# Performance work log

Measured on AMD Instinct MI355X. Metric: run time of the kernel, lower is better.

Reference implementation:

```python
import jax, jax.numpy as jnp
import numpy as np

N_NODES = 50000
N_EDGES = 800000


def setup_inputs() -> dict:
    key = jax.random.key(0)
    ks = jax.random.split(key, 8)
    feats = jax.random.normal(ks[0], (N_NODES, 256), dtype=jnp.float32)
    src = jax.random.randint(ks[1], (N_EDGES,), 0, N_NODES, dtype=jnp.int32)
    dst = jax.random.randint(ks[2], (N_EDGES,), 0, N_NODES, dtype=jnp.int32)
    # Glorot-ish init for GraphConv weights
    W0 = jax.random.normal(ks[3], (256, 256), dtype=jnp.float32) * (1.0 / 16.0)
    W1 = jax.random.normal(ks[4], (256, 256), dtype=jnp.float32) * (1.0 / 16.0)
    W2 = jax.random.normal(ks[5], (256, 128), dtype=jnp.float32) * (1.0 / 16.0)
    b0 = jnp.zeros((256,), dtype=jnp.float32)
    b1 = jnp.zeros((256,), dtype=jnp.float32)
    b2 = jnp.zeros((128,), dtype=jnp.float32)
    return {"feats": feats, "src": src, "dst": dst,
            "W0": W0, "b0": b0, "W1": W1, "b1": b1, "W2": W2, "b2": b2}


def _graph_conv(x, src, dst, W, b, activate):
    """DGL GraphConv with norm='both': h = D_in^{-1/2} A D_out^{-1/2} x W + b."""
    n = x.shape[0]
    e_ones = jnp.ones(src.shape[0], dtype=x.dtype)
    deg_out = jax.ops.segment_sum(e_ones, src, num_segments=n)  # out-degree (src norm)
    deg_in = jax.ops.segment_sum(e_ones, dst, num_segments=n)   # in-degree (dst norm)
    norm_src = jnp.where(deg_out > 0, deg_out, 1.0) ** -0.5
    norm_dst = jnp.where(deg_in > 0, deg_in, 1.0) ** -0.5
    h = x * norm_src[:, None]
    # transform first (in_feats >= out_feats path in DGL) then aggregate
    h = h @ W
    m = jax.ops.segment_sum(h[src], dst, num_segments=n)  # [N, out] neighbor sum
    h = m * norm_dst[:, None] + b
    if activate:
        h = jax.nn.relu(h)
    return h


def reference(feats, src, dst, W0, b0, W1, b1, W2, b2):
    # dropout is identity in eval mode
    h0 = _graph_conv(feats, src, dst, W0, b0, True)
    h1 = _graph_conv(h0, src, dst, W1, b1, True)
    h2 = _graph_conv(h1, src, dst, W2, b2, False)  # last layer: no activation
    return (h0, h1, h2, h2)  # (h_list..., h)
```

## Files before the change

### kernel.cpp

```cpp
#include <hip/hip_runtime.h>
#include <hip/hip_bf16.h>

#define NN 50000
#define NE 800000
#define MPAD 50048
#define BSTR 64

typedef __attribute__((ext_vector_type(8))) short short8;
typedef __attribute__((ext_vector_type(4))) float f32x4;
typedef __attribute__((ext_vector_type(4))) unsigned short us4;
typedef __attribute__((ext_vector_type(8))) unsigned short us8;

static __device__ __forceinline__ unsigned short f2bf(float f) {
    union { float f; unsigned int u; } v; v.f = f;
    unsigned int u = v.u;
    return (unsigned short)((u + 0x7FFFu + ((u >> 16) & 1u)) >> 16);
}
static __device__ __forceinline__ float bf2f(unsigned short h) {
    union { unsigned int u; float f; } v; v.u = ((unsigned int)h) << 16;
    return v.f;
}

__global__ void k_degsortW(const int* __restrict__ src, const int* __restrict__ dst,
                           int* __restrict__ degO, int* __restrict__ degI,
                           unsigned short* __restrict__ bucket,
                           const float* __restrict__ W0, const float* __restrict__ W1,
                           const float* __restrict__ W2,
                           unsigned short* __restrict__ W0T, unsigned short* __restrict__ W1T,
                           unsigned short* __restrict__ W2T) {
    int bid = blockIdx.x;
    int t = threadIdx.x;
    if (bid < NE / 256) {
        int e = bid * 256 + t;
        int s = src[e], d = dst[e];
        atomicAdd(&degO[s], 1);
        int p = atomicAdd(&degI[d], 1);
        bucket[d * BSTR + p] = (unsigned short)s;
    } else {
        int i = (bid - NE / 256) * 256 + t;
        if (i < 65536) {
            int k = i >> 8, c = i & 255;
            W0T[c * 256 + k] = f2bf(W0[i]);
        } else if (i < 131072) {
            int j = i - 65536;
            int k = j >> 8, c = j & 255;
            W1T[c * 256 + k] = f2bf(W1[j]);
        } else {
            int j = i - 131072;
            int k = j >> 7, c = j & 127;
            W2T[c * 256 + k] = f2bf(W2[j]);
        }
    }
}

__global__ __launch_bounds__(256) void k_prep(const float* __restrict__ x,
                                              const int* __restrict__ degO,
                                              const int* __restrict__ degI,
                                              float* __restrict__ nS, float* __restrict__ nD,
                                              unsigned short* __restrict__ xb) {
    const int row = blockIdx.x * 4 + (threadIdx.x >> 6);
    const int l = threadIdx.x & 63;
    int o = degO[row];
    float ns = 1.0f / sqrtf((float)(o > 0 ? o : 1));
    if (l == 0) {
        int d = degI[row];
        nS[row] = ns;
        nD[row] = 1.0f / sqrtf((float)(d > 0 ? d : 1));
    }
    f32x4 v = *(const f32x4*)&x[(long)row * 256 + l * 4];
    us4 ob;
#pragma unroll
    for (int k = 0; k < 4; k++) ob[k] = f2bf(v[k] * ns);
    *(us4*)&xb[(long)row * 256 + l * 4] = ob;
}

__global__ __launch_bounds__(256) void k_aggb(const int* __restrict__ degI,
                                              const unsigned short* __restrict__ bucket,
                                              const unsigned short* __restrict__ xb,
                                              const float* __restrict__ nD,
                                              unsigned short* __restrict__ aggb) {
    const int node = blockIdx.x * 4 + (threadIdx.x >> 6);
    const int lane = threadIdx.x & 63;
    const int q = lane >> 4;
    const int cl = (lane & 15) * 16;
    if (node >= NN) {
        if (node < MPAD && q == 0) {
            us8 z = {0,0,0,0,0,0,0,0};
            *(us8*)&aggb[(long)node * 256 + cl] = z;
            *(us8*)&aggb[(long)node * 256 + cl + 8] = z;
        }
        return;
    }
    const int deg = degI[node];
    const int bidx = (int)bucket[node * BSTR + lane];
    float acc[16];
#pragma unroll
    for (int k = 0; k < 16; k++) acc[k] = 0.f;
    int j = 0;
    for (; j + 8 <= deg; j += 8) {
        int s0 = __shfl(bidx, j + q, 64);
        int s1 = __shfl(bidx, j + 4 + q, 64);
        const unsigned short* g0 = &xb[(long)s0 * 256 + cl];
        const unsigned short* g1 = &xb[(long)s1 * 256 + cl];
        us8 a0 = *(const us8*)g0;
        us8 a1 = *(const us8*)(g0 + 8);
        us8 b0 = *(const us8*)g1;
        us8 b1 = *(const us8*)(g1 + 8);
#pragma unroll
        for (int k = 0; k < 8; k++) {
            acc[k]     += bf2f(a0[k]) + bf2f(b0[k]);
            acc[8 + k] += bf2f(a1[k]) + bf2f(b1[k]);
        }
    }
    if (j + 4 <= deg) {
        int s0 = __shfl(bidx, j + q, 64);
        const unsigned short* g0 = &xb[(long)s0 * 256 + cl];
        us8 a0 = *(const us8*)g0;
        us8 a1 = *(const us8*)(g0 + 8);
#pragma unroll
        for (int k = 0; k < 8; k++) { acc[k] += bf2f(a0[k]); acc[8 + k] += bf2f(a1[k]); }
        j += 4;
    }
    if (j < deg) {
        int s0 = __shfl(bidx, j + q, 64);
        if (q < deg - j) {
            const unsigned short* g0 = &xb[(long)s0 * 256 + cl];
            us8 a0 = *(const us8*)g0;
            us8 a1 = *(const us8*)(g0 + 8);
#pragma unroll
            for (int k = 0; k < 8; k++) { acc[k] += bf2f(a0[k]); acc[8 + k] += bf2f(a1[k]); }
        }
    }
#pragma unroll
    for (int k = 0; k < 16; k++) acc[k] += __shfl_xor(acc[k], 16, 64);
#pragma unroll
    for (int k = 0; k < 16; k++) acc[k] += __shfl_xor(acc[k], 32, 64);
    if (q == 0) {
        float nd = nD[node];
        us8 o0, o1;
#pragma unroll
        for (int k = 0; k < 8; k++) {
            o0[k] = f2bf(acc[k] * nd);
            o1[k] = f2bf(acc[8 + k] * nd);
        }
        *(us8*)&aggb[(long)node * 256 + cl] = o0;
        *(us8*)&aggb[(long)node * 256 + cl + 8] = o1;
    }
}

template<int NOUT, int MODE>
__global__ __launch_bounds__(256) void k_gemm(const unsigned short* __restrict__ A,
                                              const unsigned short* __restrict__ BT,
                                              const float* __restrict__ bias,
                                              const float* __restrict__ nS,
                                              float* __restrict__ outF,
                                              unsigned short* __restrict__ xbn,
                                              unsigned short* __restrict__ outB) {
    __shared__ unsigned short As[128][40];
    __shared__ unsigned short Bs[128][36];
    const int bm = blockIdx.x * 128;
    const int bn = blockIdx.y * 128;
    const int tid = threadIdx.x;
    const int lane = tid & 63;
    const int w = tid >> 6;
    const int wr = w >> 1, wc = w & 1;

    f32x4 acc[4][4];
#pragma unroll
    for (int m = 0; m < 4; m++)
#pragma unroll
        for (int n = 0; n < 4; n++) acc[m][n] = (f32x4){0.f, 0.f, 0.f, 0.f};

    for (int kt = 0; kt < 256; kt += 32) {
        {
            int r = tid >> 1, c = (tid & 1) * 16;
            const unsigned short* g = &A[(long)(bm + r) * 256 + kt + c];
            *(us8*)&As[r][c]     = *(const us8*)(g);
            *(us8*)&As[r][c + 8] = *(const us8*)(g + 8);
        }
        {
            int col = tid >> 1, kh = (tid & 1) * 16;
            const unsigned short* g = &BT[(long)(bn + col) * 256 + kt + kh];
            *(us8*)&Bs[col][kh]     = *(const us8*)(g);
            *(us8*)&Bs[col][kh + 8] = *(const us8*)(g + 8);
        }
        __syncthreads();

        union U { us4 h[2]; short8 s; };
        const int kb = (lane >> 4) * 4;
        short8 af[4], bf[4];
#pragma unroll
        for (int m = 0; m < 4; m++) {
            int r = wr * 64 + m * 16 + (lane & 15);
            U u; u.h[0] = *(const us4*)&As[r][kb]; u.h[1] = *(const us4*)&As[r][kb + 16];
            af[m] = u.s;
        }
#pragma unroll
        for (int n = 0; n < 4; n++) {
            int cl = wc * 64 + n * 16 + (lane & 15);
            U u; u.h[0] = *(const us4*)&Bs[cl][kb]; u.h[1] = *(const us4*)&Bs[cl][kb + 16];
            bf[n] = u.s;
        }
#pragma unroll
        for (int m = 0; m < 4; m++)
#pragma unroll
            for (int n = 0; n < 4; n++)
                acc[m][n] = __builtin_amdgcn_mfma_f32_16x16x32_bf16(af[m], bf[n], acc[m][n], 0, 0, 0);
        __syncthreads();
    }

#pragma unroll
    for (int m = 0; m < 4; m++) {
        int rbase = bm + wr * 64 + m * 16 + (lane >> 4) * 4;
        float ns[4];
        bool in[4];
        if (MODE == 0) {
#pragma unroll
            for (int j = 0; j < 4; j++) {
                int row = rbase + j;
                in[j] = row < NN;
                ns[j] = in[j] ? nS[row] : 0.f;
            }
        }
#pragma unroll
        for (int n = 0; n < 4; n++) {
            int gc = bn + wc * 64 + n * 16 + (lane & 15);
            float bb = (MODE == 0) ? bias[gc] : 0.f;
#pragma unroll
            for (int j = 0; j < 4; j++) {
                int row = rbase + j;
                if (MODE == 0) {
                    if (in[j]) {
                        float v = fmaxf(acc[m][n][j] + bb, 0.f);
                        __builtin_nontemporal_store(v, &outF[(long)row * 256 + gc]);
                        xbn[(long)row * 256 + gc] = f2bf(v * ns[j]);
                    } else {
                        xbn[(long)row * 256 + gc] = 0;
                    }
                } else {
                    outB[(long)row * NOUT + gc] = f2bf(acc[m][n][j]);
                }
            }
        }
    }
}

__global__ __launch_bounds__(256) void k_agg2(const int* __restrict__ degI,
                                              const unsigned short* __restrict__ bucket,
                                              const unsigned short* __restrict__ hgb,
                                              const float* __restrict__ nD,
                                              const float* __restrict__ b,
                                              float* __restrict__ h2,
                                              float* __restrict__ h2b) {
    const int node = blockIdx.x * 4 + (threadIdx.x >> 6);
    const int lane = threadIdx.x & 63;
    if (node >= NN) return;
    const int q = lane >> 4;
    const int cl = (lane & 15) * 8;
    const int deg = degI[node];
    const int bidx = (int)bucket[node * BSTR + lane];
    float acc[8];
#pragma unroll
    for (int k = 0; k < 8; k++) acc[k] = 0.f;
    int j = 0;
    for (; j + 8 <= deg; j += 8) {
        int s0 = __shfl(bidx, j + q, 64);
        int s1 = __shfl(bidx, j + 4 + q, 64);
        us8 vA = *(const us8*)&hgb[(long)s0 * 128 + cl];
        us8 vB = *(const us8*)&hgb[(long)s1 * 128 + cl];
#pragma unroll
        for (int k = 0; k < 8; k++) acc[k] += bf2f(vA[k]) + bf2f(vB[k]);
    }
    if (j + 4 <= deg) {
        int s0 = __shfl(bidx, j + q, 64);
        us8 vA = *(const us8*)&hgb[(long)s0 * 128 + cl];
#pragma unroll
        for (int k = 0; k < 8; k++) acc[k] += bf2f(vA[k]);
        j += 4;
    }
    if (j < deg) {
        int s0 = __shfl(bidx, j + q, 64);
        if (q < deg - j) {
            us8 vA = *(const us8*)&hgb[(long)s0 * 128 + cl];
#pragma unroll
            for (int k = 0; k < 8; k++) acc[k] += bf2f(vA[k]);
        }
    }
#pragma unroll
    for (int k = 0; k < 8; k++) acc[k] += __shfl_xor(acc[k], 16, 64);
#pragma unroll
    for (int k = 0; k < 8; k++) acc[k] += __shfl_xor(acc[k], 32, 64);
    if (q == 0) {
        float nd = nD[node];
        f32x4 v0, v1;
#pragma unroll
        for (int k = 0; k < 4; k++) v0[k] = acc[k] * nd + b[cl + k];
#pragma unroll
        for (int k = 0; k < 4; k++) v1[k] = acc[4 + k] * nd + b[cl + 4 + k];
        __builtin_nontemporal_store(v0, (f32x4*)&h2[(long)node * 128 + cl]);
        __builtin_nontemporal_store(v1, (f32x4*)&h2[(long)node * 128 + cl + 4]);
        __builtin_nontemporal_store(v0, (f32x4*)&h2b[(long)node * 128 + cl]);
        __builtin_nontemporal_store(v1, (f32x4*)&h2b[(long)node * 128 + cl + 4]);
    }
}

extern "C" void kernel_launch(void* const* d_in, const int* in_sizes, int n_in,
                              void* d_out, int out_size, void* d_ws, size_t ws_size,
                              hipStream_t stream) {
    const float* feats = (const float*)d_in[0];
    const int*   src   = (const int*)d_in[1];
    const int*   dst   = (const int*)d_in[2];
    const float* W0 = (const float*)d_in[3];
    const float* b0 = (const float*)d_in[4];
    const float* W1 = (const float*)d_in[5];
    const float* b1 = (const float*)d_in[6];
    const float* W2 = (const float*)d_in[7];
    const float* b2 = (const float*)d_in[8];

    float* out = (float*)d_out;
    float* h0  = out;
    float* h1  = out + (long)NN * 256;
    float* h2  = out + 2L * NN * 256;
    float* h2b = out + 2L * NN * 256 + (long)NN * 128;

    char* ws = (char*)d_ws;
    size_t off = 0;
    auto alloc = [&](size_t bytes) { void* p = ws + off; off += (bytes + 255) & ~255UL; return p; };
    unsigned short* xb   = (unsigned short*)alloc((size_t)MPAD * 256 * 2);
    unsigned short* xb2  = (unsigned short*)alloc((size_t)MPAD * 256 * 2);
    unsigned short* aggb = (unsigned short*)alloc((size_t)MPAD * 256 * 2);
    unsigned short* hgb  = (unsigned short*)alloc((size_t)MPAD * 128 * 2);
    unsigned short* W0T = (unsigned short*)alloc(256 * 256 * 2);
    unsigned short* W1T = (unsigned short*)alloc(256 * 256 * 2);
    unsigned short* W2T = (unsigned short*)alloc(128 * 256 * 2);
    int*   zint   = (int*)alloc((size_t)2 * NN * 4);
    int*   degO   = zint;
    int*   degI   = zint + NN;
    float* nS     = (float*)alloc(NN * 4);
    float* nD     = (float*)alloc(NN * 4);
    unsigned short* bucket = (unsigned short*)alloc((size_t)NN * BSTR * 2);

    hipMemsetAsync(zint, 0, (size_t)2 * NN * 4, stream);
    k_degsortW<<<NE / 256 + 640, 256, 0, stream>>>(src, dst, degO, degI, bucket,
                                                   W0, W1, W2, W0T, W1T, W2T);

    k_prep<<<NN / 4, 256, 0, stream>>>(feats, degO, degI, nS, nD, xb);

    k_aggb<<<MPAD / 4, 256, 0, stream>>>(degI, bucket, xb, nD, aggb);
    k_gemm<256, 0><<<dim3(MPAD / 128, 2), 256, 0, stream>>>(aggb, W0T, b0, nS, h0, xb2, nullptr);

    k_aggb<<<MPAD / 4, 256, 0, stream>>>(degI, bucket, xb2, nD, aggb);
    k_gemm<256, 0><<<dim3(MPAD / 128, 2), 256, 0, stream>>>(aggb, W1T, b1, nS, h1, xb, nullptr);

    k_gemm<128, 1><<<dim3(MPAD / 128, 1), 256, 0, stream>>>(xb, W2T, nullptr, nullptr, nullptr, nullptr, hgb);
    k_agg2<<<(NN + 3) / 4, 256, 0, stream>>>(degI, bucket, hgb, nD, b2, h2, h2b);
}
```

Before: 328.1 us.

## Fuse feature bf16 cast into degree kernel and compute degree norms on the fly

Removes the separate k_prep launch by folding the fp32-to-bf16 feature conversion into the degree/bucket kernel as extra blocks. This drops the dependency on out-degrees at that stage. Source normalization is instead applied per gathered edge in the first aggregation via degO lookups and rsqrt, and the nS/nD arrays are replaced by inline rsqrt of degrees. The first aggregation gains extra scattered degree loads and multiplies per edge in exchange for one fewer kernel launch and one fewer pass over the features.

```diff
diff --git a/kernel.cpp b/kernel.cpp
--- a/kernel.cpp
+++ b/kernel.cpp
@@ -19,6 +19,9 @@
 static __device__ __forceinline__ float bf2f(unsigned short h) {
     union { unsigned int u; float f; } v; v.u = ((unsigned int)h) << 16;
     return v.f;
+}
+static __device__ __forceinline__ float degnorm(int d) {
+    return rsqrtf((float)(d > 0 ? d : 1));
 }
 
 __global__ void k_degsortW(const int* __restrict__ src, const int* __restrict__ dst,
@@ -27,7 +30,8 @@
                            const float* __restrict__ W0, const float* __restrict__ W1,
                            const float* __restrict__ W2,
                            unsigned short* __restrict__ W0T, unsigned short* __restrict__ W1T,
-                           unsigned short* __restrict__ W2T) {
+                           unsigned short* __restrict__ W2T,
+                           const float* __restrict__ feats, unsigned short* __restrict__ xb) {
     int bid = blockIdx.x;
     int t = threadIdx.x;
     if (bid < NE / 256) {
@@ -36,7 +40,7 @@
         atomicAdd(&degO[s], 1);
         int p = atomicAdd(&degI[d], 1);
         bucket[d * BSTR + p] = (unsigned short)s;
-    } else {
+    } else if (bid < NE / 256 + 640) {
         int i = (bid - NE / 256) * 256 + t;
         if (i < 65536) {
             int k = i >> 8, c = i & 255;
@@ -50,34 +54,22 @@
             int k = j >> 7, c = j & 127;
             W2T[c * 256 + k] = f2bf(W2[j]);
         }
-    }
-}
-
-__global__ __launch_bounds__(256) void k_prep(const float* __restrict__ x,
+    } else {
+        int row = (bid - (NE / 256 + 640)) * 4 + (t >> 6);
+        int l = t & 63;
+        f32x4 v = *(const f32x4*)&feats[(long)row * 256 + l * 4];
+        us4 ob;
+#pragma unroll
+        for (int k = 0; k < 4; k++) ob[k] = f2bf(v[k]);
+        *(us4*)&xb[(long)row * 256 + l * 4] = ob;
+    }
+}
+
+template<bool SCALE_SRC>
+__global__ __launch_bounds__(256) void k_aggb(const int* __restrict__ degI,
                                               const int* __restrict__ degO,
-                                              const int* __restrict__ degI,
-                                              float* __restrict__ nS, float* __restrict__ nD,
-                                              unsigned short* __restrict__ xb) {
-    const int row = blockIdx.x * 4 + (threadIdx.x >> 6);
-    const int l = threadIdx.x & 63;
-    int o = degO[row];
-    float ns = 1.0f / sqrtf((float)(o > 0 ? o : 1));
-    if (l == 0) {
-        int d = degI[row];
-        nS[row] = ns;
-        nD[row] = 1.0f / sqrtf((float)(d > 0 ? d : 1));
-    }
-    f32x4 v = *(const f32x4*)&x[(long)row * 256 + l * 4];
-    us4 ob;
-#pragma unroll
-    for (int k = 0; k < 4; k++) ob[k] = f2bf(v[k] * ns);
-    *(us4*)&xb[(long)row * 256 + l * 4] = ob;
-}
-
-__global__ __launch_bounds__(256) void k_aggb(const int* __restrict__ degI,
                                               const unsigned short* __restrict__ bucket,
                                               const unsigned short* __restrict__ xb,
-                                              const float* __restrict__ nD,
                                               unsigned short* __restrict__ aggb) {
     const int node = blockIdx.x * 4 + (threadIdx.x >> 6);
     const int lane = threadIdx.x & 63;
@@ -100,6 +92,8 @@
     for (; j + 8 <= deg; j += 8) {
         int s0 = __shfl(bidx, j + q, 64);
         int s1 = __shfl(bidx, j + 4 + q, 64);
+        float ns0 = 1.f, ns1 = 1.f;
+        if (SCALE_SRC) { ns0 = degnorm(degO[s0]); ns1 = degnorm(degO[s1]); }
         const unsigned short* g0 = &xb[(long)s0 * 256 + cl];
         const unsigned short* g1 = &xb[(long)s1 * 256 + cl];
         us8 a0 = *(const us8*)g0;
@@ -108,27 +102,40 @@
         us8 b1 = *(const us8*)(g1 + 8);
 #pragma unroll
         for (int k = 0; k < 8; k++) {
-            acc[k]     += bf2f(a0[k]) + bf2f(b0[k]);
-            acc[8 + k] += bf2f(a1[k]) + bf2f(b1[k]);
+            if (SCALE_SRC) {
+                acc[k]     += bf2f(a0[k]) * ns0 + bf2f(b0[k]) * ns1;
+                acc[8 + k] += bf2f(a1[k]) * ns0 + bf2f(b1[k]) * ns1;
+            } else {
+                acc[k]     += bf2f(a0[k]) + bf2f(b0[k]);
+                acc[8 + k] += bf2f(a1[k]) + bf2f(b1[k]);
+            }
         }
     }
     if (j + 4 <= deg) {
         int s0 = __shfl(bidx, j + q, 64);
+        float ns0 = SCALE_SRC ? degnorm(degO[s0]) : 1.f;
         const unsigned short* g0 = &xb[(long)s0 * 256 + cl];
         us8 a0 = *(const us8*)g0;
         us8 a1 = *(const us8*)(g0 + 8);
 #pragma unroll
-        for (int k = 0; k < 8; k++) { acc[k] += bf2f(a0[k]); acc[8 + k] += bf2f(a1[k]); }
+        for (int k = 0; k < 8; k++) {
+            acc[k]     += SCALE_SRC ? bf2f(a0[k]) * ns0 : bf2f(a0[k]);
+            acc[8 + k] += SCALE_SRC ? bf2f(a1[k]) * ns0 : bf2f(a1[k]);
+        }
         j += 4;
     }
     if (j < deg) {
         int s0 = __shfl(bidx, j + q, 64);
         if (q < deg - j) {
+            float ns0 = SCALE_SRC ? degnorm(degO[s0]) : 1.f;
             const unsigned short* g0 = &xb[(long)s0 * 256 + cl];
             us8 a0 = *(const us8*)g0;
             us8 a1 = *(const us8*)(g0 + 8);
 #pragma unroll
-            for (int k = 0; k < 8; k++) { acc[k] += bf2f(a0[k]); acc[8 + k] += bf2f(a1[k]); }
+            for (int k = 0; k < 8; k++) {
+                acc[k]     += SCALE_SRC ? bf2f(a0[k]) * ns0 : bf2f(a0[k]);
+                acc[8 + k] += SCALE_SRC ? bf2f(a1[k]) * ns0 : bf2f(a1[k]);
+            }
         }
     }
 #pragma unroll
@@ -136,7 +143,7 @@
 #pragma unroll
     for (int k = 0; k < 16; k++) acc[k] += __shfl_xor(acc[k], 32, 64);
     if (q == 0) {
-        float nd = nD[node];
+        float nd = degnorm(deg);
         us8 o0, o1;
 #pragma unroll
         for (int k = 0; k < 8; k++) {
@@ -152,7 +159,7 @@
 __global__ __launch_bounds__(256) void k_gemm(const unsigned short* __restrict__ A,
                                               const unsigned short* __restrict__ BT,
                                               const float* __restrict__ bias,
-                                              const float* __restrict__ nS,
+                                              const int* __restrict__ degO,
                                               float* __restrict__ outF,
                                               unsigned short* __restrict__ xbn,
                                               unsigned short* __restrict__ outB) {
@@ -219,7 +226,7 @@
             for (int j = 0; j < 4; j++) {
                 int row = rbase + j;
                 in[j] = row < NN;
-                ns[j] = in[j] ? nS[row] : 0.f;
+                ns[j] = in[j] ? degnorm(degO[row]) : 0.f;
             }
         }
 #pragma unroll
@@ -248,7 +255,6 @@
 __global__ __launch_bounds__(256) void k_agg2(const int* __restrict__ degI,
                                               const unsigned short* __restrict__ bucket,
                                               const unsigned short* __restrict__ hgb,
-                                              const float* __restrict__ nD,
                                               const float* __restrict__ b,
                                               float* __restrict__ h2,
                                               float* __restrict__ h2b) {
@@ -291,7 +297,7 @@
 #pragma unroll
     for (int k = 0; k < 8; k++) acc[k] += __shfl_xor(acc[k], 32, 64);
     if (q == 0) {
-        float nd = nD[node];
+        float nd = degnorm(deg);
         f32x4 v0, v1;
 #pragma unroll
         for (int k = 0; k < 4; k++) v0[k] = acc[k] * nd + b[cl + k];
@@ -336,22 +342,18 @@
     int*   zint   = (int*)alloc((size_t)2 * NN * 4);
     int*   degO   = zint;
     int*   degI   = zint + NN;
-    float* nS     = (float*)alloc(NN * 4);
-    float* nD     = (float*)alloc(NN * 4);
     unsigned short* bucket = (unsigned short*)alloc((size_t)NN * BSTR * 2);
 
     hipMemsetAsync(zint, 0, (size_t)2 * NN * 4, stream);
-    k_degsortW<<<NE / 256 + 640, 256, 0, stream>>>(src, dst, degO, degI, bucket,
-                                                   W0, W1, W2, W0T, W1T, W2T);
-
-    k_prep<<<NN / 4, 256, 0, stream>>>(feats, degO, degI, nS, nD, xb);
-
-    k_aggb<<<MPAD / 4, 256, 0, stream>>>(degI, bucket, xb, nD, aggb);
-    k_gemm<256, 0><<<dim3(MPAD / 128, 2), 256, 0, stream>>>(aggb, W0T, b0, nS, h0, xb2, nullptr);
-
-    k_aggb<<<MPAD / 4, 256, 0, stream>>>(degI, bucket, xb2, nD, aggb);
-    k_gemm<256, 0><<<dim3(MPAD / 128, 2), 256, 0, stream>>>(aggb, W1T, b1, nS, h1, xb, nullptr);
+    k_degsortW<<<NE / 256 + 640 + NN / 4, 256, 0, stream>>>(
+        src, dst, degO, degI, bucket, W0, W1, W2, W0T, W1T, W2T, feats, xb);
+
+    k_aggb<true><<<MPAD / 4, 256, 0, stream>>>(degI, degO, bucket, xb, aggb);
+    k_gemm<256, 0><<<dim3(MPAD / 128, 2), 256, 0, stream>>>(aggb, W0T, b0, degO, h0, xb2, nullptr);
+
+    k_aggb<false><<<MPAD / 4, 256, 0, stream>>>(degI, degO, bucket, xb2, aggb);
+    k_gemm<256, 0><<<dim3(MPAD / 128, 2), 256, 0, stream>>>(aggb, W1T, b1, degO, h1, xb, nullptr);
 
     k_gemm<128, 1><<<dim3(MPAD / 128, 1), 256, 0, stream>>>(xb, W2T, nullptr, nullptr, nullptr, nullptr, hgb);
-    k_agg2<<<(NN + 3) / 4, 256, 0, stream>>>(degI, bucket, hgb, nD, b2, h2, h2b);
-}
+    k_agg2<<<(NN + 3) / 4, 256, 0, stream>>>(degI, bucket, hgb, b2, h2, h2b);
+}
```

New measurement: 327.5 us. About the same (-0.2%).
